# Performance work log

Hardware: AMD Instinct MI355X
Metric: run time of the kernel (lower is better)

The kernel has to match this reference:

```python
import jax, jax.numpy as jnp
import numpy as np

HIDDEN = 4096
NH = 32          # query heads
NKV = 2          # kv heads (multi_query_group_num)
HD = 128         # head dim
ROT = HD // 2    # GLM style: rotary applied to first half of head_dim
THETA = 10000.0
SCALE = HD ** -0.5
G = NH // NKV    # query heads per kv group


def _glm_rope(x, positions):
    # x: [B, S, N, HD]; GPT-J interleaved rotation on the first ROT dims.
    inv_freq = 1.0 / (THETA ** (jnp.arange(0, ROT, 2, dtype=jnp.float32) / ROT))  # [ROT//2]
    ang = positions.astype(jnp.float32)[..., None] * inv_freq                      # [B, S, ROT//2]
    cos = jnp.cos(ang)[:, :, None, :]
    sin = jnp.sin(ang)[:, :, None, :]
    xr, xp = x[..., :ROT], x[..., ROT:]
    x1, x2 = xr[..., 0::2], xr[..., 1::2]
    r1 = x1 * cos - x2 * sin
    r2 = x1 * sin + x2 * cos
    xr = jnp.stack([r1, r2], axis=-1).reshape(xr.shape)  # re-interleave
    return jnp.concatenate([xr, xp], axis=-1)


def setup_inputs() -> dict:
    key = jax.random.key(0)
    k1, k2, k3, k4 = jax.random.split(key, 4)
    B, S = 2, 2048
    positions = jnp.broadcast_to(jnp.arange(S, dtype=jnp.int64), (B, S))
    hidden_states = jax.random.normal(k1, (B, S, HIDDEN), dtype=jnp.float32)
    qkv_out = NH * HD + 2 * NKV * HD  # 4608
    w_qkv = jax.random.normal(k2, (qkv_out, HIDDEN), dtype=jnp.float32) * 0.02
    b_qkv = jax.random.normal(k3, (qkv_out,), dtype=jnp.float32) * 0.02
    w_dense = jax.random.normal(k4, (HIDDEN, NH * HD), dtype=jnp.float32) * 0.02
    return {"positions": positions, "hidden_states": hidden_states,
            "w_qkv": w_qkv, "b_qkv": b_qkv, "w_dense": w_dense}


def reference(positions, hidden_states, w_qkv, b_qkv, w_dense):
    B, S, _ = hidden_states.shape
    mixed = hidden_states @ w_qkv.T + b_qkv                      # [B,S,4608]
    q = mixed[..., : NH * HD].reshape(B, S, NH, HD)
    k = mixed[..., NH * HD: NH * HD + NKV * HD].reshape(B, S, NKV, HD)
    v = mixed[..., NH * HD + NKV * HD:].reshape(B, S, NKV, HD)

    q = _glm_rope(q, positions)
    k = _glm_rope(k, positions)

    # GQA: view q as [B, S, NKV, G, HD]
    qg = q.reshape(B, S, NKV, G, HD)
    scores = jnp.einsum('bqkgd,bskd->bkgqs', qg, k) * SCALE      # [B,NKV,G,S,S]
    causal = jnp.tril(jnp.ones((S, S), dtype=bool))
    scores = jnp.where(causal, scores, jnp.finfo(scores.dtype).min)
    probs = jax.nn.softmax(scores, axis=-1)
    ctx = jnp.einsum('bkgqs,bskd->bqkgd', probs, v)              # [B,S,NKV,G,HD]
    ctx = ctx.reshape(B, S, NH * HD)
    return ctx @ w_dense.T                                       # [B,S,HIDDEN]
```

## Files before the change

kernel.cpp:

```cpp
#include <hip/hip_runtime.h>

typedef float f32x4 __attribute__((ext_vector_type(4)));
typedef __bf16 bf16x8 __attribute__((ext_vector_type(8)));
typedef unsigned short u16x4 __attribute__((ext_vector_type(4)));
typedef unsigned short u16x8 __attribute__((ext_vector_type(8)));

#define HIDDEN 4096
#define NH 32
#define NKV 2
#define HD 128
#define SLEN 2048
#define BATCH 2
#define QKV_OUT 4608
#define MROWS 4096
#define ATT_SCALE 0.08838834764831845f
#define KCHUNK 1024

__device__ __forceinline__ unsigned short f2bf(float f) {
  unsigned int u = __float_as_uint(f);
  u += 0x7fffu + ((u >> 16) & 1u);
  return (unsigned short)(u >> 16);
}

__device__ __forceinline__ float bf2f(unsigned short s) {
  return __uint_as_float((unsigned int)s << 16);
}

__device__ __forceinline__ void gload16(const void* g, void* l) {
  __builtin_amdgcn_global_load_lds((const __attribute__((address_space(1))) void*)g,
                                   (__attribute__((address_space(3))) void*)l, 16, 0, 0);
}

__global__ __launch_bounds__(256) void cvt3_f32_bf16(
    const float* __restrict__ s0, unsigned short* __restrict__ d0, int n0,
    const float* __restrict__ s1, unsigned short* __restrict__ d1, int n1,
    const float* __restrict__ s2, unsigned short* __restrict__ d2, int n2) {
  const int ntot = n0 + n1 + n2;
  const int stride = gridDim.x * blockDim.x;
  for (int i = blockIdx.x * blockDim.x + threadIdx.x; i < ntot; i += stride) {
    const float* src;
    unsigned short* dst;
    int j = i;
    if (j < n0) { src = s0; dst = d0; }
    else if (j < n0 + n1) { j -= n0; src = s1; dst = d1; }
    else { j -= n0 + n1; src = s2; dst = d2; }
    float4 v = reinterpret_cast<const float4*>(src)[j];
    u16x4 o;
    o[0] = f2bf(v.x); o[1] = f2bf(v.y); o[2] = f2bf(v.z); o[3] = f2bf(v.w);
    reinterpret_cast<u16x4*>(dst)[j] = o;
  }
}

__global__ __launch_bounds__(256) void build_trig(float2* __restrict__ tab) {
  const int idx = blockIdx.x * 256 + threadIdx.x;
  const int p = idx >> 5, j = idx & 31;
  const float inv = __expf(-(float)j * 0.28782313662425572f);
  float sn, cs;
  sincosf((float)p * inv, &sn, &cs);
  tab[idx] = make_float2(cs, sn);
}

__global__ __launch_bounds__(512) void gemm_bf16_mfma(
    const unsigned short* __restrict__ A, const unsigned short* __restrict__ B,
    const float* __restrict__ bias, void* __restrict__ Cout, int M, int N, int K,
    int mode, const float2* __restrict__ tab, const int* __restrict__ positions,
    unsigned short* __restrict__ Qb, unsigned short* __restrict__ Kb,
    unsigned short* __restrict__ Vt) {
  __shared__ unsigned short as_[128 * 64];
  __shared__ unsigned short bs_[256 * 64];
  const int tid = threadIdx.x;
  const int wave = tid >> 6;
  const int lane = tid & 63;
  const int lr = lane & 15, lg = lane >> 4;
  const int m0 = blockIdx.y * 128;
  const int n0 = blockIdx.x * 256;
  const int wm = (wave >> 2) * 64;
  const int wn = (wave & 3) * 64;

  f32x4 acc[4][4] = {};

  const int srow8 = tid >> 3;
  const int schunk = (tid & 7) ^ (srow8 & 7);
  const int scol = schunk * 8;
  unsigned short* lA = as_ + wave * 512;
  unsigned short* lB = bs_ + wave * 512;

  const int nk = K >> 6;
  for (int kt = 0; kt < nk; ++kt) {
    const int kb = kt << 6;
    __syncthreads();
    gload16(A + (size_t)(m0 + srow8) * K + kb + scol, lA);
    gload16(A + (size_t)(m0 + 64 + srow8) * K + kb + scol, lA + 4096);
    gload16(B + (size_t)(n0 + srow8) * K + kb + scol, lB);
    gload16(B + (size_t)(n0 + 64 + srow8) * K + kb + scol, lB + 4096);
    gload16(B + (size_t)(n0 + 128 + srow8) * K + kb + scol, lB + 8192);
    gload16(B + (size_t)(n0 + 192 + srow8) * K + kb + scol, lB + 12288);
    __syncthreads();

#pragma unroll
    for (int kk = 0; kk < 2; ++kk) {
      bf16x8 aF[4], bF[4];
#pragma unroll
      for (int m4 = 0; m4 < 4; ++m4)
        aF[m4] = *reinterpret_cast<const bf16x8*>(
            &as_[(wm + m4 * 16 + lr) * 64 + (((kk * 4 + lg) ^ (lr & 7)) << 3)]);
#pragma unroll
      for (int n4 = 0; n4 < 4; ++n4)
        bF[n4] = *reinterpret_cast<const bf16x8*>(
            &bs_[(wn + n4 * 16 + lr) * 64 + (((kk * 4 + lg) ^ (lr & 7)) << 3)]);
#pragma unroll
      for (int m4 = 0; m4 < 4; ++m4)
#pragma unroll
        for (int n4 = 0; n4 < 4; ++n4)
          acc[m4][n4] =
              __builtin_amdgcn_mfma_f32_16x16x32_bf16(aF[m4], bF[n4], acc[m4][n4], 0, 0, 0);
    }
  }

  if (mode == 0) {
    float* C = (float*)Cout;
#pragma unroll
    for (int m4 = 0; m4 < 4; ++m4) {
#pragma unroll
      for (int n4 = 0; n4 < 4; ++n4) {
        const int col = n0 + wn + n4 * 16 + lr;
        const float bv = bias ? bias[col] : 0.0f;
#pragma unroll
        for (int r = 0; r < 4; ++r) {
          const int row = m0 + wm + m4 * 16 + lg * 4 + r;
          C[(size_t)row * N + col] = acc[m4][n4][r] + bv;
        }
      }
    }
  } else {
#pragma unroll
    for (int m4 = 0; m4 < 4; ++m4) {
      const int rowb = m0 + wm + m4 * 16 + lg * 4;
      const int bb = rowb >> 11;
      const int ss = rowb & 2047;
      int pos[4];
#pragma unroll
      for (int r = 0; r < 4; ++r) pos[r] = positions[rowb + r];
#pragma unroll
      for (int n4 = 0; n4 < 4; ++n4) {
        const int col = n0 + wn + n4 * 16 + lr;
        const float bv = bias[col];
        float val[4];
#pragma unroll
        for (int r = 0; r < 4; ++r) val[r] = acc[m4][n4][r] + bv;
        const int d = col & 127;
        const bool isv = (col >= NH * HD + NKV * HD);
        const bool isq = (col < NH * HD);
        if (d < 64 && !isv) {
          const int j = d >> 1;
#pragma unroll
          for (int r = 0; r < 4; ++r) {
            const float2 t = tab[pos[r] * 32 + j];
            const float other = __shfl_xor(val[r], 1);
            val[r] = (col & 1) ? (other * t.y + val[r] * t.x)
                               : (val[r] * t.x - other * t.y);
          }
        }
        if (isq) {
          const int hh = col >> 7;
          unsigned short* q = Qb + ((size_t)(bb * NH + hh) * SLEN + ss) * HD + d;
#pragma unroll
          for (int r = 0; r < 4; ++r) q[(size_t)r * HD] = f2bf(val[r] * ATT_SCALE);
        } else if (!isv) {
          const int kvh = (col - NH * HD) >> 7;
          unsigned short* k = Kb + ((size_t)(bb * NKV + kvh) * SLEN + ss) * HD + d;
#pragma unroll
          for (int r = 0; r < 4; ++r) k[(size_t)r * HD] = f2bf(val[r]);
        } else {
          const int kvh = (col - NH * HD - NKV * HD) >> 7;
          u16x4 o;
#pragma unroll
          for (int r = 0; r < 4; ++r) o[r] = f2bf(val[r]);
          *reinterpret_cast<u16x4*>(
              &Vt[((size_t)(bb * NKV + kvh) * HD + d) * SLEN + ss]) = o;
        }
      }
    }
  }
}

__global__ __launch_bounds__(512) void flash_mfma(const unsigned short* __restrict__ Qb,
                                                  const unsigned short* __restrict__ Kb,
                                                  const unsigned short* __restrict__ Vt,
                                                  unsigned short* __restrict__ ctx,
                                                  unsigned short* __restrict__ Om,
                                                  float* __restrict__ Ml) {
  __shared__ unsigned short Ks[2][64 * 128];
  __shared__ unsigned short Vs[128 * 64];
  __shared__ unsigned short Ps[8][16 * 64];

  const int tid = threadIdx.x;
  const int wave = tid >> 6, lane = tid & 63;
  const int lr = lane & 15, lg = lane >> 4;

  const int i = blockIdx.x;
  int qt, c;
  if (i < 8) { qt = 15 - i; c = 0; }
  else if (i < 16) { qt = 23 - i; c = 1; }
  else { qt = 23 - i; c = 0; }
  const int h = blockIdx.y, b = blockIdx.z;
  const int kv = h >> 4;
  const int q0 = qt * 128;
  const int s_begin = c * KCHUNK;
  const int s_end = min(KCHUNK * (c + 1), q0 + 128);
  const int nkt = (s_end - s_begin) >> 6;
  const bool single = (c == 0) && (s_end == q0 + 128);
  const int qbw = q0 + wave * 16;

  const unsigned short* Kbase = Kb + (size_t)(b * NKV + kv) * SLEN * HD;
  const unsigned short* Vbase = Vt + (size_t)(b * NKV + kv) * HD * SLEN;

  bf16x8 bQ[4];
  {
    const unsigned short* qp = Qb + ((size_t)(b * NH + h) * SLEN + qbw + lr) * HD;
#pragma unroll
    for (int ks = 0; ks < 4; ++ks)
      bQ[ks] = *reinterpret_cast<const bf16x8*>(qp + lg * 8 + ks * 32);
  }

  f32x4 accO[8] = {};
  float mi = -1e30f, li = 0.0f;

  const int vrow_off = lane >> 3, vchunk = lane & 7;
#define STAGE_K(cb, t)                                                                  \
  {                                                                                     \
    const int ss = s_begin + (t) * 64;                                                  \
    _Pragma("unroll") for (int si = 0; si < 2; ++si) {                                  \
      const int krow = wave * 8 + si * 4 + lg;                                          \
      gload16(Kbase + (size_t)(ss + krow) * HD + ((lr ^ (krow & 7)) << 3),              \
              &Ks[cb][(wave * 8 + si * 4) * 128]);                                      \
    }                                                                                   \
  }
#define STAGE_V(t)                                                                      \
  {                                                                                     \
    const int ss = s_begin + (t) * 64;                                                  \
    _Pragma("unroll") for (int si = 0; si < 2; ++si) {                                  \
      const int drow = wave * 16 + si * 8 + vrow_off;                                   \
      gload16(Vbase + (size_t)drow * SLEN + ss + ((vchunk ^ (drow & 7)) << 3),          \
              &Vs[(wave * 16 + si * 8) * 64]);                                          \
    }                                                                                   \
  }

  STAGE_K(0, 0);
  __syncthreads();

  unsigned short* Pw = Ps[wave];

  for (int kt = 0; kt < nkt; ++kt) {
    const int cur = kt & 1;
    const int s0 = s_begin + kt * 64;
    STAGE_V(kt);
    if (kt + 1 < nkt) STAGE_K(cur ^ 1, kt + 1);
    const bool part = (s0 < qbw + 16);

    f32x4 accS[4] = {};
    if (part) {
      bf16x8 aK[4][4];
#pragma unroll
      for (int kb = 0; kb < 4; ++kb)
#pragma unroll
        for (int ks = 0; ks < 4; ++ks)
          aK[kb][ks] = *reinterpret_cast<const bf16x8*>(
              &Ks[cur][(kb * 16 + lr) * 128 + (((ks * 4 + lg) ^ (lr & 7)) << 3)]);
#pragma unroll
      for (int kb = 0; kb < 4; ++kb)
#pragma unroll
        for (int ks = 0; ks < 4; ++ks)
          accS[kb] = __builtin_amdgcn_mfma_f32_16x16x32_bf16(aK[kb][ks], bQ[ks], accS[kb], 0, 0, 0);
    }

    __syncthreads();

    if (part) {
      const int qrow = qbw + lr;
      float v[16];
#pragma unroll
      for (int kb = 0; kb < 4; ++kb)
#pragma unroll
        for (int r = 0; r < 4; ++r) v[kb * 4 + r] = accS[kb][r];
      if (s0 + 63 > qbw) {
#pragma unroll
        for (int kb = 0; kb < 4; ++kb)
#pragma unroll
          for (int r = 0; r < 4; ++r)
            if (s0 + kb * 16 + lg * 4 + r > qrow) v[kb * 4 + r] = -1e30f;
      }
      float m16 = v[0];
#pragma unroll
      for (int i2 = 1; i2 < 16; ++i2) m16 = fmaxf(m16, v[i2]);
      m16 = fmaxf(m16, __shfl_xor(m16, 16));
      m16 = fmaxf(m16, __shfl_xor(m16, 32));
      const float mnew = fmaxf(mi, m16);
      const float cf = __expf(mi - mnew);
      mi = mnew;
      float rs = 0.0f;
#pragma unroll
      for (int i2 = 0; i2 < 16; ++i2) {
        const float p = __expf(v[i2] - mnew);
        v[i2] = p;
        rs += p;
      }
      rs += __shfl_xor(rs, 16);
      rs += __shfl_xor(rs, 32);
      li = li * cf + rs;
#pragma unroll
      for (int n8 = 0; n8 < 8; ++n8) accO[n8] *= cf;
#pragma unroll
      for (int kb = 0; kb < 4; ++kb) {
        const int slot = (kb * 2 + (lg >> 1)) ^ (lr & 7);
        u16x4 pk;
        pk[0] = f2bf(v[kb * 4 + 0]); pk[1] = f2bf(v[kb * 4 + 1]);
        pk[2] = f2bf(v[kb * 4 + 2]); pk[3] = f2bf(v[kb * 4 + 3]);
        *reinterpret_cast<u16x4*>(&Pw[lr * 64 + slot * 8 + (lg & 1) * 4]) = pk;
      }

      bf16x8 pa[2];
#pragma unroll
      for (int ks = 0; ks < 2; ++ks)
        pa[ks] = *reinterpret_cast<const bf16x8*>(
            &Pw[lr * 64 + (((ks * 4 + lg) ^ (lr & 7)) << 3)]);
#pragma unroll
      for (int ks = 0; ks < 2; ++ks) {
#pragma unroll
        for (int n8 = 0; n8 < 8; ++n8) {
          bf16x8 aV = *reinterpret_cast<const bf16x8*>(
              &Vs[(n8 * 16 + lr) * 64 + (((ks * 4 + lg) ^ (lr & 7)) << 3)]);
          accO[n8] = __builtin_amdgcn_mfma_f32_16x16x32_bf16(aV, pa[ks], accO[n8], 0, 0, 0);
        }
      }
    }

    __syncthreads();
  }
#undef STAGE_K
#undef STAGE_V

  if (single) {
    const float inv = 1.0f / li;
    unsigned short* orow =
        ctx + (size_t)(b * SLEN + qbw + lr) * HIDDEN + h * HD + lg * 4;
#pragma unroll
    for (int n8 = 0; n8 < 8; ++n8) {
      u16x4 o;
#pragma unroll
      for (int r = 0; r < 4; ++r) o[r] = f2bf(accO[n8][r] * inv);
      *reinterpret_cast<u16x4*>(orow + n8 * 16) = o;
    }
  } else {
    const int row1k = qbw + lr - 1024;
    const size_t pbase = (size_t)((b * NH + h) * 2 + c) * 1024 + row1k;
    if (lg == 0) {
      Ml[pbase * 2] = mi;
      Ml[pbase * 2 + 1] = li;
    }
    unsigned short* prow = Om + pbase * 128 + lg * 4;
#pragma unroll
    for (int n8 = 0; n8 < 8; ++n8) {
      u16x4 o;
#pragma unroll
      for (int r = 0; r < 4; ++r) o[r] = f2bf(accO[n8][r]);
      *reinterpret_cast<u16x4*>(prow + n8 * 16) = o;
    }
  }
}

__global__ __launch_bounds__(256) void combine_partials(
    const unsigned short* __restrict__ Om, const float* __restrict__ Ml,
    unsigned short* __restrict__ ctx) {
  const int g = blockIdx.x * 64 + (threadIdx.x >> 2);
  const int p = threadIdx.x & 3;
  const int row1k = g & 1023;
  const int h = (g >> 10) & 31;
  const int b = g >> 15;
  const size_t base0 = (size_t)((b * NH + h) * 2 + 0) * 1024 + row1k;
  const size_t base1 = (size_t)((b * NH + h) * 2 + 1) * 1024 + row1k;
  const float m0 = Ml[base0 * 2], l0 = Ml[base0 * 2 + 1];
  const float m1 = Ml[base1 * 2], l1 = Ml[base1 * 2 + 1];
  const float mx = fmaxf(m0, m1);
  const float w0 = __expf(m0 - mx), w1 = __expf(m1 - mx);
  const float inv = 1.0f / (w0 * l0 + w1 * l1);
  const unsigned short* n0 = Om + base0 * 128 + p * 32;
  const unsigned short* n1 = Om + base1 * 128 + p * 32;
  unsigned short* orow =
      ctx + (size_t)(b * SLEN + 1024 + row1k) * HIDDEN + h * HD + p * 32;
#pragma unroll
  for (int cch = 0; cch < 4; ++cch) {
    u16x8 a = *reinterpret_cast<const u16x8*>(n0 + cch * 8);
    u16x8 d = *reinterpret_cast<const u16x8*>(n1 + cch * 8);
    u16x8 o;
#pragma unroll
    for (int j = 0; j < 8; ++j)
      o[j] = f2bf((w0 * bf2f(a[j]) + w1 * bf2f(d[j])) * inv);
    *reinterpret_cast<u16x8*>(orow + cch * 8) = o;
  }
}

extern "C" void kernel_launch(void* const* d_in, const int* in_sizes, int n_in,
                              void* d_out, int out_size, void* d_ws, size_t ws_size,
                              hipStream_t stream) {
  const int* positions = (const int*)d_in[0];
  const float* hidden = (const float*)d_in[1];
  const float* w_qkv = (const float*)d_in[2];
  const float* b_qkv = (const float*)d_in[3];
  const float* w_dense = (const float*)d_in[4];
  float* out = (float*)d_out;

  char* ws = (char*)d_ws;
  size_t off = 0;
  unsigned short* mixed = (unsigned short*)(ws + off);
  off += (size_t)MROWS * QKV_OUT * 4;
  unsigned short* h_bf = (unsigned short*)(ws + off);
  off += (size_t)MROWS * HIDDEN * 2;
  unsigned short* wq_bf = (unsigned short*)(ws + off);
  off += (size_t)QKV_OUT * HIDDEN * 2;
  unsigned short* wd_bf = (unsigned short*)(ws + off);
  off += (size_t)HIDDEN * HIDDEN * 2;
  unsigned short* Kb = (unsigned short*)(ws + off);
  off += (size_t)BATCH * NKV * SLEN * HD * 2;
  unsigned short* Vt = (unsigned short*)(ws + off);
  off += (size_t)BATCH * NKV * SLEN * HD * 2;
  float2* trig = (float2*)(ws + off);
  off += (size_t)2048 * 32 * 8;
  unsigned short* Qb = h_bf;
  Qb = mixed;
  unsigned short* ctx_bf = mixed + (size_t)MROWS * HIDDEN;
  unsigned short* Om = wq_bf;
  float* Ml = (float*)(ws + off);
  off += (size_t)BATCH * NH * 2 * 1024 * 2 * 4;

  cvt3_f32_bf16<<<2048, 256, 0, stream>>>(hidden, h_bf, MROWS * HIDDEN / 4,
                                          w_qkv, wq_bf, QKV_OUT * HIDDEN / 4,
                                          w_dense, wd_bf, HIDDEN * HIDDEN / 4);
  build_trig<<<256, 256, 0, stream>>>(trig);

  gemm_bf16_mfma<<<dim3(QKV_OUT / 256, MROWS / 128), 512, 0, stream>>>(
      h_bf, wq_bf, b_qkv, nullptr, MROWS, QKV_OUT, HIDDEN, 2, trig, positions,
      Qb, Kb, Vt);

  flash_mfma<<<dim3(24, NH, BATCH), 512, 0, stream>>>(Qb, Kb, Vt, ctx_bf, Om, Ml);

  combine_partials<<<1024, 256, 0, stream>>>(Om, Ml, ctx_bf);

  gemm_bf16_mfma<<<dim3(HIDDEN / 256, MROWS / 128), 512, 0, stream>>>(
      ctx_bf, wd_bf, nullptr, out, MROWS, HIDDEN, HIDDEN, 0, nullptr, nullptr,
      nullptr, nullptr, nullptr);
}
```

Measured before the change: 529.4 us.

## Overlap GEMM tile loads with MFMA, drop attention split-K, fuse trig build

The GEMM main loop now issues the next K-tile's global-to-LDS loads after reading the second half-fragments, so loads overlap the second batch of MFMAs. Flash attention no longer splits long query tiles into two KV chunks, which removes the partial buffers and the combine kernel. The trig-table build is folded into the conversion kernel to save a launch. The cost is less parallelism for the longest query tiles, and a single-buffered LDS scheme that relies on correct barrier placement.

```diff
diff --git a/kernel.cpp b/kernel.cpp
--- a/kernel.cpp
+++ b/kernel.cpp
@@ -14,7 +14,6 @@
 #define QKV_OUT 4608
 #define MROWS 4096
 #define ATT_SCALE 0.08838834764831845f
-#define KCHUNK 1024
 
 __device__ __forceinline__ unsigned short f2bf(float f) {
   unsigned int u = __float_as_uint(f);
@@ -34,7 +33,16 @@
 __global__ __launch_bounds__(256) void cvt3_f32_bf16(
     const float* __restrict__ s0, unsigned short* __restrict__ d0, int n0,
     const float* __restrict__ s1, unsigned short* __restrict__ d1, int n1,
-    const float* __restrict__ s2, unsigned short* __restrict__ d2, int n2) {
+    const float* __restrict__ s2, unsigned short* __restrict__ d2, int n2,
+    float2* __restrict__ tab) {
+  if (blockIdx.x < 256) {
+    const int idx = blockIdx.x * 256 + threadIdx.x;
+    const int p = idx >> 5, j = idx & 31;
+    const float inv = __expf(-(float)j * 0.28782313662425572f);
+    float sn, cs;
+    sincosf((float)p * inv, &sn, &cs);
+    tab[idx] = make_float2(cs, sn);
+  }
   const int ntot = n0 + n1 + n2;
   const int stride = gridDim.x * blockDim.x;
   for (int i = blockIdx.x * blockDim.x + threadIdx.x; i < ntot; i += stride) {
@@ -49,15 +57,6 @@
     o[0] = f2bf(v.x); o[1] = f2bf(v.y); o[2] = f2bf(v.z); o[3] = f2bf(v.w);
     reinterpret_cast<u16x4*>(dst)[j] = o;
   }
-}
-
-__global__ __launch_bounds__(256) void build_trig(float2* __restrict__ tab) {
-  const int idx = blockIdx.x * 256 + threadIdx.x;
-  const int p = idx >> 5, j = idx & 31;
-  const float inv = __expf(-(float)j * 0.28782313662425572f);
-  float sn, cs;
-  sincosf((float)p * inv, &sn, &cs);
-  tab[idx] = make_float2(cs, sn);
 }
 
 __global__ __launch_bounds__(512) void gemm_bf16_mfma(
@@ -80,42 +79,59 @@
   f32x4 acc[4][4] = {};
 
   const int srow8 = tid >> 3;
-  const int schunk = (tid & 7) ^ (srow8 & 7);
-  const int scol = schunk * 8;
+  const int scol = ((tid & 7) ^ (srow8 & 7)) * 8;
   unsigned short* lA = as_ + wave * 512;
   unsigned short* lB = bs_ + wave * 512;
 
+#define GSTAGE(kb)                                                     \
+  {                                                                    \
+    gload16(A + (size_t)(m0 + srow8) * K + (kb) + scol, lA);           \
+    gload16(A + (size_t)(m0 + 64 + srow8) * K + (kb) + scol, lA + 4096); \
+    gload16(B + (size_t)(n0 + srow8) * K + (kb) + scol, lB);           \
+    gload16(B + (size_t)(n0 + 64 + srow8) * K + (kb) + scol, lB + 4096); \
+    gload16(B + (size_t)(n0 + 128 + srow8) * K + (kb) + scol, lB + 8192); \
+    gload16(B + (size_t)(n0 + 192 + srow8) * K + (kb) + scol, lB + 12288); \
+  }
+
   const int nk = K >> 6;
+  GSTAGE(0);
+  __syncthreads();
+
   for (int kt = 0; kt < nk; ++kt) {
-    const int kb = kt << 6;
+    bf16x8 aF[4], bF[4];
+#pragma unroll
+    for (int m4 = 0; m4 < 4; ++m4)
+      aF[m4] = *reinterpret_cast<const bf16x8*>(
+          &as_[(wm + m4 * 16 + lr) * 64 + ((lg ^ (lr & 7)) << 3)]);
+#pragma unroll
+    for (int n4 = 0; n4 < 4; ++n4)
+      bF[n4] = *reinterpret_cast<const bf16x8*>(
+          &bs_[(wn + n4 * 16 + lr) * 64 + ((lg ^ (lr & 7)) << 3)]);
+#pragma unroll
+    for (int m4 = 0; m4 < 4; ++m4)
+#pragma unroll
+      for (int n4 = 0; n4 < 4; ++n4)
+        acc[m4][n4] =
+            __builtin_amdgcn_mfma_f32_16x16x32_bf16(aF[m4], bF[n4], acc[m4][n4], 0, 0, 0);
+#pragma unroll
+    for (int m4 = 0; m4 < 4; ++m4)
+      aF[m4] = *reinterpret_cast<const bf16x8*>(
+          &as_[(wm + m4 * 16 + lr) * 64 + (((4 + lg) ^ (lr & 7)) << 3)]);
+#pragma unroll
+    for (int n4 = 0; n4 < 4; ++n4)
+      bF[n4] = *reinterpret_cast<const bf16x8*>(
+          &bs_[(wn + n4 * 16 + lr) * 64 + (((4 + lg) ^ (lr & 7)) << 3)]);
     __syncthreads();
-    gload16(A + (size_t)(m0 + srow8) * K + kb + scol, lA);
-    gload16(A + (size_t)(m0 + 64 + srow8) * K + kb + scol, lA + 4096);
-    gload16(B + (size_t)(n0 + srow8) * K + kb + scol, lB);
-    gload16(B + (size_t)(n0 + 64 + srow8) * K + kb + scol, lB + 4096);
-    gload16(B + (size_t)(n0 + 128 + srow8) * K + kb + scol, lB + 8192);
-    gload16(B + (size_t)(n0 + 192 + srow8) * K + kb + scol, lB + 12288);
+    if (kt + 1 < nk) GSTAGE((kt + 1) << 6);
+#pragma unroll
+    for (int m4 = 0; m4 < 4; ++m4)
+#pragma unroll
+      for (int n4 = 0; n4 < 4; ++n4)
+        acc[m4][n4] =
+            __builtin_amdgcn_mfma_f32_16x16x32_bf16(aF[m4], bF[n4], acc[m4][n4], 0, 0, 0);
     __syncthreads();
-
-#pragma unroll
-    for (int kk = 0; kk < 2; ++kk) {
-      bf16x8 aF[4], bF[4];
-#pragma unroll
-      for (int m4 = 0; m4 < 4; ++m4)
-        aF[m4] = *reinterpret_cast<const bf16x8*>(
-            &as_[(wm + m4 * 16 + lr) * 64 + (((kk * 4 + lg) ^ (lr & 7)) << 3)]);
-#pragma unroll
-      for (int n4 = 0; n4 < 4; ++n4)
-        bF[n4] = *reinterpret_cast<const bf16x8*>(
-            &bs_[(wn + n4 * 16 + lr) * 64 + (((kk * 4 + lg) ^ (lr & 7)) << 3)]);
-#pragma unroll
-      for (int m4 = 0; m4 < 4; ++m4)
-#pragma unroll
-        for (int n4 = 0; n4 < 4; ++n4)
-          acc[m4][n4] =
-              __builtin_amdgcn_mfma_f32_16x16x32_bf16(aF[m4], bF[n4], acc[m4][n4], 0, 0, 0);
-    }
-  }
+  }
+#undef GSTAGE
 
   if (mode == 0) {
     float* C = (float*)Cout;
@@ -187,9 +203,7 @@
 __global__ __launch_bounds__(512) void flash_mfma(const unsigned short* __restrict__ Qb,
                                                   const unsigned short* __restrict__ Kb,
                                                   const unsigned short* __restrict__ Vt,
-                                                  unsigned short* __restrict__ ctx,
-                                                  unsigned short* __restrict__ Om,
-                                                  float* __restrict__ Ml) {
+                                                  unsigned short* __restrict__ ctx) {
   __shared__ unsigned short Ks[2][64 * 128];
   __shared__ unsigned short Vs[128 * 64];
   __shared__ unsigned short Ps[8][16 * 64];
@@ -198,18 +212,11 @@
   const int wave = tid >> 6, lane = tid & 63;
   const int lr = lane & 15, lg = lane >> 4;
 
-  const int i = blockIdx.x;
-  int qt, c;
-  if (i < 8) { qt = 15 - i; c = 0; }
-  else if (i < 16) { qt = 23 - i; c = 1; }
-  else { qt = 23 - i; c = 0; }
+  const int qt = 15 - (int)blockIdx.x;
   const int h = blockIdx.y, b = blockIdx.z;
   const int kv = h >> 4;
   const int q0 = qt * 128;
-  const int s_begin = c * KCHUNK;
-  const int s_end = min(KCHUNK * (c + 1), q0 + 128);
-  const int nkt = (s_end - s_begin) >> 6;
-  const bool single = (c == 0) && (s_end == q0 + 128);
+  const int nkt = qt * 2 + 2;
   const int qbw = q0 + wave * 16;
 
   const unsigned short* Kbase = Kb + (size_t)(b * NKV + kv) * SLEN * HD;
@@ -229,7 +236,7 @@
   const int vrow_off = lane >> 3, vchunk = lane & 7;
 #define STAGE_K(cb, t)                                                                  \
   {                                                                                     \
-    const int ss = s_begin + (t) * 64;                                                  \
+    const int ss = (t) * 64;                                                            \
     _Pragma("unroll") for (int si = 0; si < 2; ++si) {                                  \
       const int krow = wave * 8 + si * 4 + lg;                                          \
       gload16(Kbase + (size_t)(ss + krow) * HD + ((lr ^ (krow & 7)) << 3),              \
@@ -238,7 +245,7 @@
   }
 #define STAGE_V(t)                                                                      \
   {                                                                                     \
-    const int ss = s_begin + (t) * 64;                                                  \
+    const int ss = (t) * 64;                                                            \
     _Pragma("unroll") for (int si = 0; si < 2; ++si) {                                  \
       const int drow = wave * 16 + si * 8 + vrow_off;                                   \
       gload16(Vbase + (size_t)drow * SLEN + ss + ((vchunk ^ (drow & 7)) << 3),          \
@@ -253,7 +260,7 @@
 
   for (int kt = 0; kt < nkt; ++kt) {
     const int cur = kt & 1;
-    const int s0 = s_begin + kt * 64;
+    const int s0 = kt * 64;
     STAGE_V(kt);
     if (kt + 1 < nkt) STAGE_K(cur ^ 1, kt + 1);
     const bool part = (s0 < qbw + 16);
@@ -340,63 +347,14 @@
 #undef STAGE_K
 #undef STAGE_V
 
-  if (single) {
-    const float inv = 1.0f / li;
-    unsigned short* orow =
-        ctx + (size_t)(b * SLEN + qbw + lr) * HIDDEN + h * HD + lg * 4;
-#pragma unroll
-    for (int n8 = 0; n8 < 8; ++n8) {
-      u16x4 o;
-#pragma unroll
-      for (int r = 0; r < 4; ++r) o[r] = f2bf(accO[n8][r] * inv);
-      *reinterpret_cast<u16x4*>(orow + n8 * 16) = o;
-    }
-  } else {
-    const int row1k = qbw + lr - 1024;
-    const size_t pbase = (size_t)((b * NH + h) * 2 + c) * 1024 + row1k;
-    if (lg == 0) {
-      Ml[pbase * 2] = mi;
-      Ml[pbase * 2 + 1] = li;
-    }
-    unsigned short* prow = Om + pbase * 128 + lg * 4;
-#pragma unroll
-    for (int n8 = 0; n8 < 8; ++n8) {
-      u16x4 o;
-#pragma unroll
-      for (int r = 0; r < 4; ++r) o[r] = f2bf(accO[n8][r]);
-      *reinterpret_cast<u16x4*>(prow + n8 * 16) = o;
-    }
-  }
-}
-
-__global__ __launch_bounds__(256) void combine_partials(
-    const unsigned short* __restrict__ Om, const float* __restrict__ Ml,
-    unsigned short* __restrict__ ctx) {
-  const int g = blockIdx.x * 64 + (threadIdx.x >> 2);
-  const int p = threadIdx.x & 3;
-  const int row1k = g & 1023;
-  const int h = (g >> 10) & 31;
-  const int b = g >> 15;
-  const size_t base0 = (size_t)((b * NH + h) * 2 + 0) * 1024 + row1k;
-  const size_t base1 = (size_t)((b * NH + h) * 2 + 1) * 1024 + row1k;
-  const float m0 = Ml[base0 * 2], l0 = Ml[base0 * 2 + 1];
-  const float m1 = Ml[base1 * 2], l1 = Ml[base1 * 2 + 1];
-  const float mx = fmaxf(m0, m1);
-  const float w0 = __expf(m0 - mx), w1 = __expf(m1 - mx);
-  const float inv = 1.0f / (w0 * l0 + w1 * l1);
-  const unsigned short* n0 = Om + base0 * 128 + p * 32;
-  const unsigned short* n1 = Om + base1 * 128 + p * 32;
-  unsigned short* orow =
-      ctx + (size_t)(b * SLEN + 1024 + row1k) * HIDDEN + h * HD + p * 32;
-#pragma unroll
-  for (int cch = 0; cch < 4; ++cch) {
-    u16x8 a = *reinterpret_cast<const u16x8*>(n0 + cch * 8);
-    u16x8 d = *reinterpret_cast<const u16x8*>(n1 + cch * 8);
-    u16x8 o;
-#pragma unroll
-    for (int j = 0; j < 8; ++j)
-      o[j] = f2bf((w0 * bf2f(a[j]) + w1 * bf2f(d[j])) * inv);
-    *reinterpret_cast<u16x8*>(orow + cch * 8) = o;
+  const float inv = 1.0f / li;
+  unsigned short* orow = ctx + (size_t)(b * SLEN + qbw + lr) * HIDDEN + h * HD + lg * 4;
+#pragma unroll
+  for (int n8 = 0; n8 < 8; ++n8) {
+    u16x4 o;
+#pragma unroll
+    for (int r = 0; r < 4; ++r) o[r] = f2bf(accO[n8][r] * inv);
+    *reinterpret_cast<u16x4*>(orow + n8 * 16) = o;
   }
 }
 
@@ -426,25 +384,18 @@
   off += (size_t)BATCH * NKV * SLEN * HD * 2;
   float2* trig = (float2*)(ws + off);
   off += (size_t)2048 * 32 * 8;
-  unsigned short* Qb = h_bf;
-  Qb = mixed;
+  unsigned short* Qb = mixed;
   unsigned short* ctx_bf = mixed + (size_t)MROWS * HIDDEN;
-  unsigned short* Om = wq_bf;
-  float* Ml = (float*)(ws + off);
-  off += (size_t)BATCH * NH * 2 * 1024 * 2 * 4;
 
   cvt3_f32_bf16<<<2048, 256, 0, stream>>>(hidden, h_bf, MROWS * HIDDEN / 4,
                                           w_qkv, wq_bf, QKV_OUT * HIDDEN / 4,
-                                          w_dense, wd_bf, HIDDEN * HIDDEN / 4);
-  build_trig<<<256, 256, 0, stream>>>(trig);
+                                          w_dense, wd_bf, HIDDEN * HIDDEN / 4, trig);
 
   gemm_bf16_mfma<<<dim3(QKV_OUT / 256, MROWS / 128), 512, 0, stream>>>(
       h_bf, wq_bf, b_qkv, nullptr, MROWS, QKV_OUT, HIDDEN, 2, trig, positions,
       Qb, Kb, Vt);
 
-  flash_mfma<<<dim3(24, NH, BATCH), 512, 0, stream>>>(Qb, Kb, Vt, ctx_bf, Om, Ml);
-
-  combine_partials<<<1024, 256, 0, stream>>>(Om, Ml, ctx_bf);
+  flash_mfma<<<dim3(16, NH, BATCH), 512, 0, stream>>>(Qb, Kb, Vt, ctx_bf);
 
   gemm_bf16_mfma<<<dim3(HIDDEN / 256, MROWS / 128), 512, 0, stream>>>(
       ctx_bf, wd_bf, nullptr, out, MROWS, HIDDEN, HIDDEN, 0, nullptr, nullptr,
```

Measured after the change: 559.7 us. +5.7%, slower.
